# Performance work log

Measured on AMD Instinct MI355X. Metric: run time of the kernel, lower is better.

## Reference

```python
import jax, jax.numpy as jnp
import numpy as np
import math

B, L, S = 2, 2048, 2048
DIN, DK, DV, DOUT, H = 512, 512, 512, 512, 8
HEAD_SIZE = DK / H  # attention_head_size = dim_key_query_all / num_attention_heads


def setup_inputs() -> dict:
    key = jax.random.key(0)
    ks = jax.random.split(key, 12)
    inv = 1.0 / math.sqrt(DIN)
    return {
        "queries": jax.random.normal(ks[0], (B, L, DIN), jnp.float32),
        "keys": jax.random.normal(ks[1], (B, S, DIN), jnp.float32),
        "values": jax.random.normal(ks[2], (B, S, DIN), jnp.float32),
        "attn_mask": 0,
        "Wq": jax.random.uniform(ks[3], (DK, DIN), jnp.float32, -inv, inv),
        "Wk": jax.random.uniform(ks[4], (DK, DIN), jnp.float32, -inv, inv),
        "Wv": jax.random.uniform(ks[5], (DV, DIN), jnp.float32, -inv, inv),
        "bv": jax.random.uniform(ks[6], (DV,), jnp.float32, -inv, inv),
        "Wcb": jax.random.uniform(ks[7], (H, DIN), jnp.float32, -inv, inv),
        "mixing": 0.2 * jax.random.normal(ks[8], (H, DK), jnp.float32),
        "Wd": jax.random.uniform(ks[9], (DOUT, DV), jnp.float32, -1.0 / math.sqrt(DV), 1.0 / math.sqrt(DV)),
        "bd": jax.random.uniform(ks[10], (DOUT,), jnp.float32, -1.0 / math.sqrt(DV), 1.0 / math.sqrt(DV)),
    }


def reference(queries, keys, values, attn_mask, Wq, Wk, Wv, bv, Wcb, mixing, Wd, bd):
    # projections
    q = jnp.einsum('bld,ed->ble', queries, Wq)            # [B,L,DK]
    k = jnp.einsum('bsd,ed->bse', keys, Wk)               # [B,S,DK]
    v = jnp.einsum('bsd,ed->bse', values, Wv) + bv        # [B,S,DV]
    v = v.reshape(B, S, H, DV // H).transpose(0, 2, 1, 3)  # [B,H,S,dv]
    # collaborative scores: (q * mixing_h) @ k^T, per head
    mixed_q = q[:, None, :, :] * mixing[None, :, None, :]  # [B,H,L,DK]
    scores = jnp.einsum('bhle,bse->bhls', mixed_q, k)      # [B,H,L,S]
    # content bias: keys -> [B,S,H] -> broadcast over queries
    cb = jnp.einsum('bsd,hd->bhs', keys, Wcb)              # [B,H,S]
    scores = (scores + cb[:, :, None, :]) / math.sqrt(HEAD_SIZE)
    probs = jax.nn.softmax(scores, axis=-1)                # dropout p=0 (eval)
    ctx = jnp.einsum('bhls,bhsv->bhlv', probs, v)          # [B,H,L,dv]
    ctx = ctx.transpose(0, 2, 1, 3).reshape(B, L, DV)      # [B,L,DV]
    out = jnp.einsum('blv,ov->blo', ctx, Wd) + bd          # [B,L,DOUT]
    return out, probs
```

## Files before the change

kernel.cpp:

```cpp
#include <hip/hip_runtime.h>

typedef unsigned short u16;
typedef __bf16 bf16x8 __attribute__((ext_vector_type(8)));
typedef float floatx4 __attribute__((ext_vector_type(4)));

#define B_ 2
#define L_ 2048
#define S_ 2048
#define D_ 512
#define H_ 8

static __device__ __forceinline__ u16 f2bf(float f) {
  union { float f; unsigned u; } v; v.f = f;
  unsigned u = v.u;
  return (u16)((u + 0x7FFFu + ((u >> 16) & 1u)) >> 16);
}
static __device__ __forceinline__ float bf2f(u16 h) {
  union { unsigned u; float f; } v; v.u = ((unsigned)h) << 16;
  return v.f;
}

__global__ __launch_bounds__(256) void qkv_gemm(
    const float* __restrict__ Qin, const float* __restrict__ Kin, const float* __restrict__ Vin,
    const float* __restrict__ Wq, const float* __restrict__ Wk, const float* __restrict__ Wv,
    const float* __restrict__ bv,
    u16* __restrict__ qo, u16* __restrict__ ko, u16* __restrict__ vo)
{
  __shared__ u16 As[128][72];
  __shared__ u16 Bs[128][72];
  const int z = blockIdx.z;
  const float* A = (z == 0) ? Qin : (z == 1) ? Kin : Vin;
  const float* W = (z == 0) ? Wq : (z == 1) ? Wk : Wv;
  const int tid = threadIdx.x;
  const int m0 = blockIdx.y * 128;
  const int n0 = blockIdx.x * 128;
  const int lane = tid & 63, w = tid >> 6;
  const int ml = lane & 15, kl = lane >> 4;
  const int mqw = (w >> 1) * 64, nq = (w & 1) * 64;
  const int srow = tid >> 4, scg = tid & 15;

  floatx4 acc[4][4] = {};

  for (int k0 = 0; k0 < 512; k0 += 64) {
#pragma unroll
    for (int i = 0; i < 8; ++i) {
      const int r = srow + i * 16;
      float4 av = *(const float4*)&A[(size_t)(m0 + r) * 512 + k0 + scg * 4];
      ushort4 ua; ua.x = f2bf(av.x); ua.y = f2bf(av.y); ua.z = f2bf(av.z); ua.w = f2bf(av.w);
      *(ushort4*)&As[r][scg * 4] = ua;
      float4 wv = *(const float4*)&W[(size_t)(n0 + r) * 512 + k0 + scg * 4];
      ushort4 uw; uw.x = f2bf(wv.x); uw.y = f2bf(wv.y); uw.z = f2bf(wv.z); uw.w = f2bf(wv.w);
      *(ushort4*)&Bs[r][scg * 4] = uw;
    }
    __syncthreads();
#pragma unroll
    for (int kk = 0; kk < 64; kk += 32) {
      bf16x8 af[4], bfv[4];
#pragma unroll
      for (int i = 0; i < 4; ++i) af[i] = *(const bf16x8*)&As[mqw + i * 16 + ml][kk + kl * 8];
#pragma unroll
      for (int j = 0; j < 4; ++j) bfv[j] = *(const bf16x8*)&Bs[nq + j * 16 + ml][kk + kl * 8];
#pragma unroll
      for (int i = 0; i < 4; ++i)
#pragma unroll
        for (int j = 0; j < 4; ++j)
          acc[i][j] = __builtin_amdgcn_mfma_f32_16x16x32_bf16(af[i], bfv[j], acc[i][j], 0, 0, 0);
    }
    __syncthreads();
  }
#pragma unroll
  for (int i = 0; i < 4; ++i)
#pragma unroll
    for (int j = 0; j < 4; ++j) {
      const int gc = n0 + nq + j * 16 + ml;
#pragma unroll
      for (int r = 0; r < 4; ++r) {
        const int gr = m0 + mqw + i * 16 + kl * 4 + r;
        float v = acc[i][j][r];
        if (z == 0)      qo[(size_t)gr * 512 + gc] = f2bf(v);
        else if (z == 1) ko[(size_t)gr * 512 + gc] = f2bf(v);
        else             vo[(size_t)gr * 512 + gc] = f2bf(v + bv[gc]);
      }
    }
}

__global__ __launch_bounds__(256) void mixq_kernel(
    const u16* __restrict__ qb, const float* __restrict__ mixing, u16* __restrict__ mq)
{
  __shared__ float mixs[8 * 512];
  const int tid = threadIdx.x;
#pragma unroll
  for (int i = 0; i < 4; ++i)
    *(float4*)&mixs[(tid + i * 256) * 4] = *(const float4*)&mixing[(tid + i * 256) * 4];
  __syncthreads();
  const size_t unit = (size_t)blockIdx.x * 256 + tid;
  const size_t el = unit * 8;
  const int e = (int)(el & 511);
  const size_t bl = el >> 9;
  const int b = (int)(bl >> 11);
  const int l = (int)(bl & 2047);
  uint4 qv = *(const uint4*)&qb[el];
  const float q0 = bf2f((u16)(qv.x & 0xFFFFu)), q1 = bf2f((u16)(qv.x >> 16));
  const float q2 = bf2f((u16)(qv.y & 0xFFFFu)), q3 = bf2f((u16)(qv.y >> 16));
  const float q4 = bf2f((u16)(qv.z & 0xFFFFu)), q5 = bf2f((u16)(qv.z >> 16));
  const float q6 = bf2f((u16)(qv.w & 0xFFFFu)), q7 = bf2f((u16)(qv.w >> 16));
#pragma unroll
  for (int h = 0; h < 8; ++h) {
    const float* mp = &mixs[h * 512 + e];
    uint4 o;
    o.x = (unsigned)f2bf(q0 * mp[0]) | ((unsigned)f2bf(q1 * mp[1]) << 16);
    o.y = (unsigned)f2bf(q2 * mp[2]) | ((unsigned)f2bf(q3 * mp[3]) << 16);
    o.z = (unsigned)f2bf(q4 * mp[4]) | ((unsigned)f2bf(q5 * mp[5]) << 16);
    o.w = (unsigned)f2bf(q6 * mp[6]) | ((unsigned)f2bf(q7 * mp[7]) << 16);
    *(uint4*)&mq[(((size_t)b * 8 + h) * 2048 + l) * 512 + e] = o;
  }
}

__global__ __launch_bounds__(256) void out_gemm(
    const float* __restrict__ A, const float* __restrict__ W,
    const float* __restrict__ bias, float* __restrict__ out)
{
  __shared__ u16 As[128][72];
  __shared__ u16 Bs[128][72];
  const int tid = threadIdx.x;
  const int m0 = blockIdx.y * 128;
  const int n0 = blockIdx.x * 128;
  const int lane = tid & 63, w = tid >> 6;
  const int ml = lane & 15, kl = lane >> 4;
  const int mqw = (w >> 1) * 64, nq = (w & 1) * 64;
  const int srow = tid >> 4, scg = tid & 15;

  floatx4 acc[4][4] = {};

  for (int k0 = 0; k0 < 512; k0 += 64) {
#pragma unroll
    for (int i = 0; i < 8; ++i) {
      const int r = srow + i * 16;
      float4 av = *(const float4*)&A[(size_t)(m0 + r) * 512 + k0 + scg * 4];
      ushort4 ua; ua.x = f2bf(av.x); ua.y = f2bf(av.y); ua.z = f2bf(av.z); ua.w = f2bf(av.w);
      *(ushort4*)&As[r][scg * 4] = ua;
      float4 wv = *(const float4*)&W[(size_t)(n0 + r) * 512 + k0 + scg * 4];
      ushort4 uw; uw.x = f2bf(wv.x); uw.y = f2bf(wv.y); uw.z = f2bf(wv.z); uw.w = f2bf(wv.w);
      *(ushort4*)&Bs[r][scg * 4] = uw;
    }
    __syncthreads();
#pragma unroll
    for (int kk = 0; kk < 64; kk += 32) {
      bf16x8 af[4], bfv[4];
#pragma unroll
      for (int i = 0; i < 4; ++i) af[i] = *(const bf16x8*)&As[mqw + i * 16 + ml][kk + kl * 8];
#pragma unroll
      for (int j = 0; j < 4; ++j) bfv[j] = *(const bf16x8*)&Bs[nq + j * 16 + ml][kk + kl * 8];
#pragma unroll
      for (int i = 0; i < 4; ++i)
#pragma unroll
        for (int j = 0; j < 4; ++j)
          acc[i][j] = __builtin_amdgcn_mfma_f32_16x16x32_bf16(af[i], bfv[j], acc[i][j], 0, 0, 0);
    }
    __syncthreads();
  }
#pragma unroll
  for (int i = 0; i < 4; ++i)
#pragma unroll
    for (int j = 0; j < 4; ++j) {
      const int gc = n0 + nq + j * 16 + ml;
#pragma unroll
      for (int r = 0; r < 4; ++r) {
        const int gr = m0 + mqw + i * 16 + kl * 4 + r;
        out[(size_t)gr * 512 + gc] = acc[i][j][r] + bias[gc];
      }
    }
}

__global__ __launch_bounds__(256) void cb_kernel(
    const float* __restrict__ keys, const float* __restrict__ Wcb, float* __restrict__ cbuf)
{
  __shared__ float Wl[8 * 512];
  const int tid = threadIdx.x;
#pragma unroll
  for (int i = 0; i < 4; ++i) {
    const int idx = tid + i * 256;
    *(float4*)&Wl[idx * 4] = *(const float4*)&Wcb[idx * 4];
  }
  __syncthreads();
  const int w = tid >> 6, lane = tid & 63;
  const int rowid = blockIdx.x * 4 + w;
  const int b = rowid >> 11, s = rowid & 2047;
  const float* kr = keys + (size_t)rowid * 512;
  float acc[8] = {0.f, 0.f, 0.f, 0.f, 0.f, 0.f, 0.f, 0.f};
  for (int e = lane; e < 512; e += 64) {
    const float kv = kr[e];
#pragma unroll
    for (int hh = 0; hh < 8; ++hh) acc[hh] += kv * Wl[hh * 512 + e];
  }
#pragma unroll
  for (int hh = 0; hh < 8; ++hh) {
#pragma unroll
    for (int off = 32; off > 0; off >>= 1) acc[hh] += __shfl_xor(acc[hh], off, 64);
  }
  if (lane == 0) {
#pragma unroll
    for (int hh = 0; hh < 8; ++hh)
      cbuf[((size_t)b * 8 + hh) * 2048 + s] = acc[hh];
  }
}

__global__ __launch_bounds__(256) void transpose_v(
    const u16* __restrict__ vb, u16* __restrict__ vT)
{
  __shared__ u16 t[64][72];
  const int tid = threadIdx.x;
  const int e0 = blockIdx.x * 64;
  const int s0 = blockIdx.y * 64;
  const int b = blockIdx.z;
  const int rr = tid >> 3, g = tid & 7;
#pragma unroll
  for (int i = 0; i < 2; ++i) {
    const int r = rr + i * 32;
    *(uint4*)&t[r][g * 8] = *(const uint4*)&vb[((size_t)b * S_ + s0 + r) * 512 + e0 + g * 8];
  }
  __syncthreads();
#pragma unroll
  for (int i = 0; i < 2; ++i) {
    const int er = rr + i * 32;
    uint4 o;
    o.x = (unsigned)t[g * 8 + 0][er] | ((unsigned)t[g * 8 + 1][er] << 16);
    o.y = (unsigned)t[g * 8 + 2][er] | ((unsigned)t[g * 8 + 3][er] << 16);
    o.z = (unsigned)t[g * 8 + 4][er] | ((unsigned)t[g * 8 + 5][er] << 16);
    o.w = (unsigned)t[g * 8 + 6][er] | ((unsigned)t[g * 8 + 7][er] << 16);
    *(uint4*)&vT[((size_t)b * 512 + e0 + er) * S_ + s0 + g * 8] = o;
  }
}

template<int BF16OUT>
__global__ __launch_bounds__(256) void scores_gemm(
    const u16* __restrict__ mq, const u16* __restrict__ kb,
    const float* __restrict__ cbuf, float* __restrict__ sc, u16* __restrict__ sb)
{
  __shared__ u16 As[128][72];
  __shared__ u16 Bs[128][72];
  const int tid = threadIdx.x;
  const int bh = blockIdx.z, b = bh >> 3;
  const int m0 = blockIdx.y * 128;
  const int n0 = blockIdx.x * 128;
  const u16* mqb = mq + (size_t)bh * L_ * 512;
  const u16* kbb = kb + (size_t)b * S_ * 512;
  const int lane = tid & 63, w = tid >> 6;
  const int ml = lane & 15, kl = lane >> 4;
  const int mqw = (w >> 1) * 64, nq = (w & 1) * 64;
  const int brow = tid >> 3, bcg = tid & 7;

  floatx4 acc[4][4] = {};

  for (int k0 = 0; k0 < 512; k0 += 64) {
#pragma unroll
    for (int i = 0; i < 4; ++i) {
      const int r = brow + i * 32;
      *(uint4*)&As[r][bcg * 8] = *(const uint4*)&mqb[(size_t)(m0 + r) * 512 + k0 + bcg * 8];
      *(uint4*)&Bs[r][bcg * 8] = *(const uint4*)&kbb[(size_t)(n0 + r) * 512 + k0 + bcg * 8];
    }
    __syncthreads();
#pragma unroll
    for (int kk = 0; kk < 64; kk += 32) {
      bf16x8 af[4], bfv[4];
#pragma unroll
      for (int i = 0; i < 4; ++i) af[i] = *(const bf16x8*)&As[mqw + i * 16 + ml][kk + kl * 8];
#pragma unroll
      for (int j = 0; j < 4; ++j) bfv[j] = *(const bf16x8*)&Bs[nq + j * 16 + ml][kk + kl * 8];
#pragma unroll
      for (int i = 0; i < 4; ++i)
#pragma unroll
        for (int j = 0; j < 4; ++j)
          acc[i][j] = __builtin_amdgcn_mfma_f32_16x16x32_bf16(af[i], bfv[j], acc[i][j], 0, 0, 0);
    }
    __syncthreads();
  }
  if constexpr (BF16OUT) {
    u16* outp = sb + ((size_t)bh * L_ + m0) * S_ + n0;
#pragma unroll
    for (int j = 0; j < 4; ++j) {
      const int gcl = nq + j * 16 + ml;
      const float cbv = cbuf[(size_t)bh * S_ + n0 + gcl];
#pragma unroll
      for (int i = 0; i < 4; ++i)
#pragma unroll
        for (int r = 0; r < 4; ++r) {
          const int grl = mqw + i * 16 + kl * 4 + r;
          outp[(size_t)grl * S_ + gcl] = f2bf((acc[i][j][r] + cbv) * 0.125f);
        }
    }
  } else {
    float* outp = sc + ((size_t)bh * L_ + m0) * S_ + n0;
#pragma unroll
    for (int j = 0; j < 4; ++j) {
      const int gcl = nq + j * 16 + ml;
      const float cbv = cbuf[(size_t)bh * S_ + n0 + gcl];
#pragma unroll
      for (int i = 0; i < 4; ++i)
#pragma unroll
        for (int r = 0; r < 4; ++r) {
          const int grl = mqw + i * 16 + kl * 4 + r;
          outp[(size_t)grl * S_ + gcl] = (acc[i][j][r] + cbv) * 0.125f;
        }
    }
  }
}

template<int BF16IN>
__global__ __launch_bounds__(256) void softmax_stream(
    const u16* __restrict__ sb, float* probs)
{
  const int tid = threadIdx.x;
  const int row = blockIdx.x * 4 + (tid >> 6);
  const int lane = tid & 63;
  float s[32];
  if constexpr (BF16IN) {
    const u16* rp = sb + (size_t)row * 2048;
#pragma unroll
    for (int j = 0; j < 8; ++j) {
      uint2 v = *(const uint2*)&rp[lane * 4 + j * 256];
      s[4 * j + 0] = bf2f((u16)(v.x & 0xFFFFu));
      s[4 * j + 1] = bf2f((u16)(v.x >> 16));
      s[4 * j + 2] = bf2f((u16)(v.y & 0xFFFFu));
      s[4 * j + 3] = bf2f((u16)(v.y >> 16));
    }
  } else {
    const float* rp = probs + (size_t)row * 2048;
#pragma unroll
    for (int j = 0; j < 8; ++j) {
      float4 v = *(const float4*)&rp[lane * 4 + j * 256];
      s[4 * j + 0] = v.x; s[4 * j + 1] = v.y; s[4 * j + 2] = v.z; s[4 * j + 3] = v.w;
    }
  }
  float m = -3.0e38f;
#pragma unroll
  for (int i = 0; i < 32; ++i) m = fmaxf(m, s[i]);
#pragma unroll
  for (int off = 32; off > 0; off >>= 1) m = fmaxf(m, __shfl_xor(m, off, 64));
  float s0 = 0.f, s1 = 0.f, s2 = 0.f, s3 = 0.f;
#pragma unroll
  for (int i = 0; i < 32; i += 4) {
    s[i + 0] = __expf(s[i + 0] - m); s0 += s[i + 0];
    s[i + 1] = __expf(s[i + 1] - m); s1 += s[i + 1];
    s[i + 2] = __expf(s[i + 2] - m); s2 += s[i + 2];
    s[i + 3] = __expf(s[i + 3] - m); s3 += s[i + 3];
  }
  float sum = (s0 + s1) + (s2 + s3);
#pragma unroll
  for (int off = 32; off > 0; off >>= 1) sum += __shfl_xor(sum, off, 64);
  const float rl = 1.0f / sum;
  float* op = probs + (size_t)row * 2048;
#pragma unroll
  for (int j = 0; j < 8; ++j) {
    float4 o;
    o.x = s[4 * j + 0] * rl; o.y = s[4 * j + 1] * rl;
    o.z = s[4 * j + 2] * rl; o.w = s[4 * j + 3] * rl;
    *(float4*)&op[lane * 4 + j * 256] = o;
  }
}

__global__ __launch_bounds__(256) void ctx_gemm(
    const float* __restrict__ probs, const u16* __restrict__ vT, float* __restrict__ ctx)
{
  __shared__ u16 As[64][72];
  __shared__ u16 Bs[64][72];
  const int tid = threadIdx.x;
  const int bh = blockIdx.z, b = bh >> 3, h = bh & 7;
  const int m0 = blockIdx.x * 64;
  const int kz = blockIdx.y;
  const float* Ap = probs + ((size_t)bh * L_ + m0) * S_;
  const u16* Bp = vT + ((size_t)b * 512 + h * 64) * S_;
  const int lane = tid & 63, w = tid >> 6;
  const int ml = lane & 15, kl = lane >> 4;
  const int srow = tid >> 4, scg = tid & 15;
  const int brow = tid >> 3, bcg = tid & 7;

  floatx4 acc[4] = {};

  const int kend = kz * 1024 + 1024;
  for (int k0 = kz * 1024; k0 < kend; k0 += 64) {
#pragma unroll
    for (int i = 0; i < 4; ++i) {
      const int r = srow + i * 16;
      float4 av = *(const float4*)&Ap[(size_t)r * S_ + k0 + scg * 4];
      ushort4 ua; ua.x = f2bf(av.x); ua.y = f2bf(av.y); ua.z = f2bf(av.z); ua.w = f2bf(av.w);
      *(ushort4*)&As[r][scg * 4] = ua;
    }
#pragma unroll
    for (int i = 0; i < 2; ++i) {
      const int r = brow + i * 32;
      *(uint4*)&Bs[r][bcg * 8] = *(const uint4*)&Bp[(size_t)r * S_ + k0 + bcg * 8];
    }
    __syncthreads();
#pragma unroll
    for (int kk = 0; kk < 64; kk += 32) {
      bf16x8 af = *(const bf16x8*)&As[w * 16 + ml][kk + kl * 8];
#pragma unroll
      for (int j = 0; j < 4; ++j) {
        bf16x8 bfv = *(const bf16x8*)&Bs[j * 16 + ml][kk + kl * 8];
        acc[j] = __builtin_amdgcn_mfma_f32_16x16x32_bf16(af, bfv, acc[j], 0, 0, 0);
      }
    }
    __syncthreads();
  }
#pragma unroll
  for (int j = 0; j < 4; ++j) {
    const int gc = h * 64 + j * 16 + ml;
#pragma unroll
    for (int r = 0; r < 4; ++r) {
      const int gl = m0 + w * 16 + kl * 4 + r;
      atomicAdd(&ctx[((size_t)b * L_ + gl) * 512 + gc], acc[j][r]);
    }
  }
}

__global__ __launch_bounds__(256) void zero_ctx(float* __restrict__ p)
{
  const size_t i = ((size_t)blockIdx.x * 256 + threadIdx.x) * 4;
  float4 z; z.x = 0.f; z.y = 0.f; z.z = 0.f; z.w = 0.f;
  *(float4*)&p[i] = z;
}

extern "C" void kernel_launch(void* const* d_in, const int* in_sizes, int n_in,
                              void* d_out, int out_size, void* d_ws, size_t ws_size,
                              hipStream_t stream) {
  const float* queries = (const float*)d_in[0];
  const float* keys    = (const float*)d_in[1];
  const float* values  = (const float*)d_in[2];
  const float* Wq  = (const float*)d_in[4];
  const float* Wk  = (const float*)d_in[5];
  const float* Wv  = (const float*)d_in[6];
  const float* bv  = (const float*)d_in[7];
  const float* Wcb = (const float*)d_in[8];
  const float* mixing = (const float*)d_in[9];
  const float* Wd  = (const float*)d_in[10];
  const float* bd  = (const float*)d_in[11];

  float* out   = (float*)d_out;
  float* probs = out + (size_t)B_ * L_ * 512;

  char* ws = (char*)d_ws;
  u16*   qb  = (u16*)(ws);
  u16*   kb  = (u16*)(ws + (size_t)4  * 1024 * 1024);
  u16*   vb  = (u16*)(ws + (size_t)8  * 1024 * 1024);
  u16*   vT  = (u16*)(ws + (size_t)12 * 1024 * 1024);
  float* cbuf= (float*)(ws + (size_t)16 * 1024 * 1024);
  float* ctx = (float*)(ws + (size_t)17 * 1024 * 1024);
  u16*   mq  = (u16*)(ws + (size_t)25 * 1024 * 1024);
  const size_t SB16_OFF = (size_t)57 * 1024 * 1024;
  const size_t SB16_SZ  = (size_t)B_ * H_ * L_ * S_ * 2;
  u16* sb16 = (u16*)(ws + SB16_OFF);
  const bool bigws = (ws_size >= SB16_OFF + SB16_SZ);

  hipLaunchKernelGGL(qkv_gemm, dim3(4, 32, 3), dim3(256), 0, stream,
                     queries, keys, values, Wq, Wk, Wv, bv, qb, kb, vb);
  hipLaunchKernelGGL(mixq_kernel, dim3(1024), dim3(256), 0, stream, qb, mixing, mq);
  hipLaunchKernelGGL(cb_kernel, dim3(1024), dim3(256), 0, stream, keys, Wcb, cbuf);
  hipLaunchKernelGGL(transpose_v, dim3(8, 32, 2), dim3(256), 0, stream, vb, vT);
  hipLaunchKernelGGL(zero_ctx, dim3(2048), dim3(256), 0, stream, ctx);
  if (bigws) {
    hipLaunchKernelGGL(HIP_KERNEL_NAME(scores_gemm<1>), dim3(16, 16, 16), dim3(256), 0, stream,
                       mq, kb, cbuf, probs, sb16);
    hipLaunchKernelGGL(HIP_KERNEL_NAME(softmax_stream<1>), dim3(8192), dim3(256), 0, stream,
                       sb16, probs);
  } else {
    hipLaunchKernelGGL(HIP_KERNEL_NAME(scores_gemm<0>), dim3(16, 16, 16), dim3(256), 0, stream,
                       mq, kb, cbuf, probs, sb16);
    hipLaunchKernelGGL(HIP_KERNEL_NAME(softmax_stream<0>), dim3(8192), dim3(256), 0, stream,
                       sb16, probs);
  }
  hipLaunchKernelGGL(ctx_gemm, dim3(32, 2, 16), dim3(256), 0, stream, probs, vT, ctx);
  hipLaunchKernelGGL(out_gemm, dim3(4, 32, 1), dim3(256), 0, stream,
                     ctx, Wd, bd, out);
}
```

Before: 586.6 us.

## Write bf16 probs in softmax, use global_load_lds, drop split-K atomics

Softmax now also writes a bf16 copy of the probabilities into the scratch buffer, so ctx_gemm reads half the bytes and skips the fp32-to-bf16 conversion. The scores and ctx GEMMs load tiles with direct global-to-LDS 16-byte loads, which removes the row padding. ctx_gemm no longer splits K, so the atomics and the zero_ctx launch go away, at the cost of half as many blocks. Removing the padding may add LDS bank conflicts on fragment reads, and the extra bf16 write costs softmax bandwidth.

```diff
diff --git a/kernel.cpp b/kernel.cpp
--- a/kernel.cpp
+++ b/kernel.cpp
@@ -18,6 +18,12 @@
 static __device__ __forceinline__ float bf2f(u16 h) {
   union { unsigned u; float f; } v; v.u = ((unsigned)h) << 16;
   return v.f;
+}
+
+static __device__ __forceinline__ void gload16(const void* g, void* l) {
+  __builtin_amdgcn_global_load_lds(
+      (const __attribute__((address_space(1))) void*)g,
+      (__attribute__((address_space(3))) void*)l, 16, 0, 0);
 }
 
 __global__ __launch_bounds__(256) void qkv_gemm(
@@ -237,8 +243,8 @@
     const u16* __restrict__ mq, const u16* __restrict__ kb,
     const float* __restrict__ cbuf, float* __restrict__ sc, u16* __restrict__ sb)
 {
-  __shared__ u16 As[128][72];
-  __shared__ u16 Bs[128][72];
+  __shared__ u16 As[128][64];
+  __shared__ u16 Bs[128][64];
   const int tid = threadIdx.x;
   const int bh = blockIdx.z, b = bh >> 3;
   const int m0 = blockIdx.y * 128;
@@ -248,16 +254,18 @@
   const int lane = tid & 63, w = tid >> 6;
   const int ml = lane & 15, kl = lane >> 4;
   const int mqw = (w >> 1) * 64, nq = (w & 1) * 64;
-  const int brow = tid >> 3, bcg = tid & 7;
+  const int lr = lane >> 3;
+  const int lc = (lane & 7) * 8;
 
   floatx4 acc[4][4] = {};
 
   for (int k0 = 0; k0 < 512; k0 += 64) {
 #pragma unroll
     for (int i = 0; i < 4; ++i) {
-      const int r = brow + i * 32;
-      *(uint4*)&As[r][bcg * 8] = *(const uint4*)&mqb[(size_t)(m0 + r) * 512 + k0 + bcg * 8];
-      *(uint4*)&Bs[r][bcg * 8] = *(const uint4*)&kbb[(size_t)(n0 + r) * 512 + k0 + bcg * 8];
+      const int c = w * 4 + i;
+      const int r = c * 8 + lr;
+      gload16(&mqb[(size_t)(m0 + r) * 512 + k0 + lc], &As[c * 8][0]);
+      gload16(&kbb[(size_t)(n0 + r) * 512 + k0 + lc], &Bs[c * 8][0]);
     }
     __syncthreads();
 #pragma unroll
@@ -308,7 +316,7 @@
 
 template<int BF16IN>
 __global__ __launch_bounds__(256) void softmax_stream(
-    const u16* __restrict__ sb, float* probs)
+    u16* __restrict__ sb, float* probs)
 {
   const int tid = threadIdx.x;
   const int row = blockIdx.x * 4 + (tid >> 6);
@@ -350,46 +358,65 @@
   for (int off = 32; off > 0; off >>= 1) sum += __shfl_xor(sum, off, 64);
   const float rl = 1.0f / sum;
   float* op = probs + (size_t)row * 2048;
+  u16* bp = sb + (size_t)row * 2048;
 #pragma unroll
   for (int j = 0; j < 8; ++j) {
     float4 o;
     o.x = s[4 * j + 0] * rl; o.y = s[4 * j + 1] * rl;
     o.z = s[4 * j + 2] * rl; o.w = s[4 * j + 3] * rl;
     *(float4*)&op[lane * 4 + j * 256] = o;
-  }
-}
-
+    if constexpr (BF16IN) {
+      uint2 t;
+      t.x = (unsigned)f2bf(o.x) | ((unsigned)f2bf(o.y) << 16);
+      t.y = (unsigned)f2bf(o.z) | ((unsigned)f2bf(o.w) << 16);
+      *(uint2*)&bp[lane * 4 + j * 256] = t;
+    }
+  }
+}
+
+template<int BF16IN>
 __global__ __launch_bounds__(256) void ctx_gemm(
-    const float* __restrict__ probs, const u16* __restrict__ vT, float* __restrict__ ctx)
-{
-  __shared__ u16 As[64][72];
-  __shared__ u16 Bs[64][72];
-  const int tid = threadIdx.x;
-  const int bh = blockIdx.z, b = bh >> 3, h = bh & 7;
+    const float* __restrict__ probsf, const u16* __restrict__ pb,
+    const u16* __restrict__ vT, float* __restrict__ ctx)
+{
+  __shared__ u16 As[64][64];
+  __shared__ u16 Bs[64][64];
+  const int tid = threadIdx.x;
+  const int bh = blockIdx.y, b = bh >> 3, h = bh & 7;
   const int m0 = blockIdx.x * 64;
-  const int kz = blockIdx.y;
-  const float* Ap = probs + ((size_t)bh * L_ + m0) * S_;
-  const u16* Bp = vT + ((size_t)b * 512 + h * 64) * S_;
   const int lane = tid & 63, w = tid >> 6;
   const int ml = lane & 15, kl = lane >> 4;
-  const int srow = tid >> 4, scg = tid & 15;
-  const int brow = tid >> 3, bcg = tid & 7;
+  const int lr = lane >> 3;
+  const int lc = (lane & 7) * 8;
+  const u16* Ap = pb + ((size_t)bh * L_ + m0) * S_;
+  const u16* Bp = vT + ((size_t)b * 512 + h * 64) * S_;
 
   floatx4 acc[4] = {};
 
-  const int kend = kz * 1024 + 1024;
-  for (int k0 = kz * 1024; k0 < kend; k0 += 64) {
-#pragma unroll
-    for (int i = 0; i < 4; ++i) {
-      const int r = srow + i * 16;
-      float4 av = *(const float4*)&Ap[(size_t)r * S_ + k0 + scg * 4];
-      ushort4 ua; ua.x = f2bf(av.x); ua.y = f2bf(av.y); ua.z = f2bf(av.z); ua.w = f2bf(av.w);
-      *(ushort4*)&As[r][scg * 4] = ua;
-    }
-#pragma unroll
-    for (int i = 0; i < 2; ++i) {
-      const int r = brow + i * 32;
-      *(uint4*)&Bs[r][bcg * 8] = *(const uint4*)&Bp[(size_t)r * S_ + k0 + bcg * 8];
+  for (int k0 = 0; k0 < 2048; k0 += 64) {
+    if constexpr (BF16IN) {
+#pragma unroll
+      for (int i = 0; i < 2; ++i) {
+        const int c = w * 2 + i;
+        const int r = c * 8 + lr;
+        gload16(&Ap[(size_t)r * S_ + k0 + lc], &As[c * 8][0]);
+        gload16(&Bp[(size_t)r * S_ + k0 + lc], &Bs[c * 8][0]);
+      }
+    } else {
+      const int srow = tid >> 4, scg = tid & 15;
+#pragma unroll
+      for (int i = 0; i < 4; ++i) {
+        const int r = srow + i * 16;
+        float4 av = *(const float4*)&probsf[((size_t)bh * L_ + m0 + r) * S_ + k0 + scg * 4];
+        ushort4 ua; ua.x = f2bf(av.x); ua.y = f2bf(av.y); ua.z = f2bf(av.z); ua.w = f2bf(av.w);
+        *(ushort4*)&As[r][scg * 4] = ua;
+      }
+#pragma unroll
+      for (int i = 0; i < 2; ++i) {
+        const int c = w * 2 + i;
+        const int r = c * 8 + lr;
+        gload16(&Bp[(size_t)r * S_ + k0 + lc], &Bs[c * 8][0]);
+      }
     }
     __syncthreads();
 #pragma unroll
@@ -409,16 +436,9 @@
 #pragma unroll
     for (int r = 0; r < 4; ++r) {
       const int gl = m0 + w * 16 + kl * 4 + r;
-      atomicAdd(&ctx[((size_t)b * L_ + gl) * 512 + gc], acc[j][r]);
-    }
-  }
-}
-
-__global__ __launch_bounds__(256) void zero_ctx(float* __restrict__ p)
-{
-  const size_t i = ((size_t)blockIdx.x * 256 + threadIdx.x) * 4;
-  float4 z; z.x = 0.f; z.y = 0.f; z.z = 0.f; z.w = 0.f;
-  *(float4*)&p[i] = z;
+      ctx[((size_t)b * L_ + gl) * 512 + gc] = acc[j][r];
+    }
+  }
 }
 
 extern "C" void kernel_launch(void* const* d_in, const int* in_sizes, int n_in,
@@ -457,19 +477,21 @@
   hipLaunchKernelGGL(mixq_kernel, dim3(1024), dim3(256), 0, stream, qb, mixing, mq);
   hipLaunchKernelGGL(cb_kernel, dim3(1024), dim3(256), 0, stream, keys, Wcb, cbuf);
   hipLaunchKernelGGL(transpose_v, dim3(8, 32, 2), dim3(256), 0, stream, vb, vT);
-  hipLaunchKernelGGL(zero_ctx, dim3(2048), dim3(256), 0, stream, ctx);
   if (bigws) {
     hipLaunchKernelGGL(HIP_KERNEL_NAME(scores_gemm<1>), dim3(16, 16, 16), dim3(256), 0, stream,
                        mq, kb, cbuf, probs, sb16);
     hipLaunchKernelGGL(HIP_KERNEL_NAME(softmax_stream<1>), dim3(8192), dim3(256), 0, stream,
                        sb16, probs);
+    hipLaunchKernelGGL(HIP_KERNEL_NAME(ctx_gemm<1>), dim3(32, 16), dim3(256), 0, stream,
+                       probs, sb16, vT, ctx);
   } else {
     hipLaunchKernelGGL(HIP_KERNEL_NAME(scores_gemm<0>), dim3(16, 16, 16), dim3(256), 0, stream,
                        mq, kb, cbuf, probs, sb16);
     hipLaunchKernelGGL(HIP_KERNEL_NAME(softmax_stream<0>), dim3(8192), dim3(256), 0, stream,
                        sb16, probs);
-  }
-  hipLaunchKernelGGL(ctx_gemm, dim3(32, 2, 16), dim3(256), 0, stream, probs, vT, ctx);
+    hipLaunchKernelGGL(HIP_KERNEL_NAME(ctx_gemm<0>), dim3(32, 16), dim3(256), 0, stream,
+                       probs, sb16, vT, ctx);
+  }
   hipLaunchKernelGGL(out_gemm, dim3(4, 32, 1), dim3(256), 0, stream,
                      ctx, Wd, bd, out);
 }
```

After: 579.6 us. No clear change (-1.2%).
